# Optimization experiments

Hardware: AMD Instinct MI355X
Metric: run time of the kernel (lower is better)

## Reference

```python
import jax, jax.numpy as jnp
import numpy as np

B, L, D = 8, 2048, 64

def setup_inputs() -> dict:
    key = jax.random.key(0)
    kq, kk, kv, kqm, kkm = jax.random.split(key, 5)
    return {
        "query": jax.random.normal(kq, (B, L, D), dtype=jnp.float32),
        "key": jax.random.normal(kk, (B, L, D), dtype=jnp.float32),
        "value": jax.random.normal(kv, (B, L, D), dtype=jnp.float32),
        "q_mask": jax.random.randint(kqm, (B, L), 0, 2, dtype=jnp.int32),
        "k_mask": jax.random.randint(kkm, (B, L), 0, 2, dtype=jnp.int32),
    }

def reference(query, key, value, q_mask, k_mask):
    # scale defaults to D_q; divide scores by sqrt(D_q)
    D_q = query.shape[-1]
    qm = q_mask.astype(jnp.float32)  # [B, L_q]
    km = k_mask.astype(jnp.float32)  # [B, L_k]
    # outer-product mask: [B, L_q, L_k]
    mask = qm[:, :, None] * km[:, None, :]
    scores = jnp.einsum("bqd,bkd->bqk", query, key) / jnp.sqrt(jnp.float32(D_q))
    # masked_fill(-inf).exp(): masked positions become exactly 0
    A = jnp.where(mask == 0, 0.0, jnp.exp(scores))  # [B, L_q, L_k]
    # sum clamped to min 1.0 (NOT a standard softmax normalization)
    A_sum = jnp.maximum(A.sum(axis=-1, keepdims=True), 1.0)
    attn = A / A_sum
    return jnp.einsum("bqk,bkd->bqd", attn, value)
```

## Files before the change

### kernel.cpp

```cpp
#include <hip/hip_runtime.h>
#include <hip/hip_bf16.h>
#include <stdint.h>

#define BB 8
#define LL 2048
#define DD 64

typedef short bf16x8 __attribute__((ext_vector_type(8)));
typedef float f32x4 __attribute__((ext_vector_type(4)));
typedef unsigned short ushort_t;
typedef __attribute__((address_space(1))) const unsigned int gas_u32;
typedef __attribute__((address_space(3))) unsigned int las_u32;

__device__ __forceinline__ unsigned pk2(float lo, float hi) {
    union { __hip_bfloat162 h; unsigned u; } c;
    c.h = __float22bfloat162_rn(make_float2(lo, hi));
    return c.u;
}
__device__ __forceinline__ float4 ld4(const float* __restrict__ p) {
    return *reinterpret_cast<const float4*>(p);
}
__device__ __forceinline__ bf16x8 cvt8f(float4 a, float4 b) {
    union { bf16x8 v; unsigned u[4]; } r;
    r.u[0] = pk2(a.x, a.y); r.u[1] = pk2(a.z, a.w);
    r.u[2] = pk2(b.x, b.y); r.u[3] = pk2(b.z, b.w);
    return r.v;
}
__device__ __forceinline__ void glds16(const void* g, void* lds_base_uniform) {
    __builtin_amdgcn_global_load_lds((gas_u32*)g, (las_u32*)lds_base_uniform, 16, 0, 0);
}
__device__ __forceinline__ float bfu2f(unsigned bits) {
    union { unsigned u; float f; } c; c.u = bits << 16; return c.f;
}
__device__ __forceinline__ unsigned f2bf_u(float f) {
    union { float f; unsigned u; } v; v.f = f;
    return (v.u + 0x8000u) >> 16;
}
__device__ __forceinline__ bf16x8 cvt8(const float* __restrict__ p) {
    float4 a = ld4(p), b = ld4(p + 4);
    union { bf16x8 v; unsigned u[4]; } r;
    r.u[0] = f2bf_u(a.x) | (f2bf_u(a.y) << 16);
    r.u[1] = f2bf_u(a.z) | (f2bf_u(a.w) << 16);
    r.u[2] = f2bf_u(b.x) | (f2bf_u(b.y) << 16);
    r.u[3] = f2bf_u(b.z) | (f2bf_u(b.w) << 16);
    return r.v;
}

__global__ __launch_bounds__(256) void pack_k_bf16(const float* __restrict__ K,
                                                   ushort_t* __restrict__ Kb) {
    size_t i = ((size_t)blockIdx.x * 256 + threadIdx.x) * 8;
    float4 a = ld4(K + i), b = ld4(K + i + 4);
    uint4 o = { pk2(a.x, a.y), pk2(a.z, a.w), pk2(b.x, b.y), pk2(b.z, b.w) };
    *reinterpret_cast<uint4*>(Kb + i) = o;
}

__global__ __launch_bounds__(256) void transpose_v_bf(const float* __restrict__ V,
                                                      ushort_t* __restrict__ VT) {
    __shared__ float t[64][65];
    const int b  = blockIdx.x >> 5;
    const int kt = (blockIdx.x & 31) << 6;
    {
        const int r  = threadIdx.x >> 2;
        const int cq = (threadIdx.x & 3) << 4;
        const float* src = V + ((size_t)(b * LL + kt + r)) * DD + cq;
        #pragma unroll
        for (int i = 0; i < 4; ++i) {
            float4 v = ld4(src + 4 * i);
            t[r][cq + 4 * i + 0] = v.x; t[r][cq + 4 * i + 1] = v.y;
            t[r][cq + 4 * i + 2] = v.z; t[r][cq + 4 * i + 3] = v.w;
        }
    }
    __syncthreads();
    {
        const int d  = threadIdx.x >> 2;
        const int kq = (threadIdx.x & 3) << 4;
        ushort_t* dst = VT + ((size_t)(b * DD + d)) * LL + kt + kq;
        #pragma unroll
        for (int u = 0; u < 2; ++u) {
            uint4 o;
            o.x = pk2(t[kq + 8 * u + 0][d], t[kq + 8 * u + 1][d]);
            o.y = pk2(t[kq + 8 * u + 2][d], t[kq + 8 * u + 3][d]);
            o.z = pk2(t[kq + 8 * u + 4][d], t[kq + 8 * u + 5][d]);
            o.w = pk2(t[kq + 8 * u + 6][d], t[kq + 8 * u + 7][d]);
            *reinterpret_cast<uint4*>(dst + 8 * u) = o;
        }
    }
}

__global__ __launch_bounds__(512, 4) void attn7(
    const float* __restrict__ Q,
    const ushort_t* __restrict__ Kbf,
    const ushort_t* __restrict__ VTb,
    const int* __restrict__ qmask,
    const int* __restrict__ kmask,
    float* __restrict__ Out)
{
    const int tid  = threadIdx.x;
    const int wave = tid >> 6;
    const int lane = tid & 63;
    const int ln   = lane & 15;
    const int quad = lane >> 4;
    const int s    = wave >> 2;
    const int h    = wave & 3;

    const int b  = blockIdx.x >> 6;
    const int q0 = (blockIdx.x & 63) << 5;

    __shared__ char     lds[2][32768];
    __shared__ ushort_t kmbf[LL];
    __shared__ float    Osum[32][68];
    __shared__ float    Dsum[32];

    const char* Kg = (const char*)Kbf + (size_t)b * LL * DD * 2;
    const char* Vg = (const char*)VTb + (size_t)b * DD * LL * 2;
    const int krow1 = wave * 8 + (lane >> 3);
    const int kscol = (lane & 7) ^ (lane >> 3);
    const int vd1   = wave * 4 + (lane >> 4);
    const int vscol = (lane & 15) ^ (vd1 & 15);

    #define STAGE(buf, k0)                                                      \
        do {                                                                    \
            glds16(Kg + (size_t)((k0) + krow1) * 128 + kscol * 16,              \
                   &lds[buf][wave * 1024]);                                     \
            glds16(Kg + (size_t)((k0) + krow1 + 64) * 128 + kscol * 16,         \
                   &lds[buf][(wave + 8) * 1024]);                               \
            glds16(Vg + (size_t)vd1 * (LL * 2) + (k0) * 2 + vscol * 16,         \
                   &lds[buf][16384 + wave * 1024]);                             \
            glds16(Vg + (size_t)(vd1 + 32) * (LL * 2) + (k0) * 2 + vscol * 16,  \
                   &lds[buf][16384 + (wave + 8) * 1024]);                       \
        } while (0)

    STAGE(0, 0);

    for (int i = tid; i < 32 * 68; i += 512) (&Osum[0][0])[i] = 0.f;
    if (tid < 32) Dsum[tid] = 0.f;
    {
        int4 a = *reinterpret_cast<const int4*>(kmask + b * LL + tid * 4);
        uint2 u;
        u.x = (a.x ? 0x3F80u : 0u) | ((a.y ? 0x3F80u : 0u) << 16);
        u.y = (a.z ? 0x3F80u : 0u) | ((a.w ? 0x3F80u : 0u) << 16);
        *reinterpret_cast<uint2*>(kmbf + tid * 4) = u;
    }
    bf16x8 qf[2];
    {
        const float* qp = Q + ((size_t)(b * LL + q0 + 16 * s + ln)) * DD + quad * 8;
        qf[0] = cvt8f(ld4(qp),      ld4(qp + 4));
        qf[1] = cvt8f(ld4(qp + 32), ld4(qp + 36));
    }

    f32x4 Oacc[4] = {{0,0,0,0},{0,0,0,0},{0,0,0,0},{0,0,0,0}};
    float dsum = 0.f;

    const int src0 = ln + ((quad & 1) << 5);
    const int src1 = src0 + 16;
    const bool hi  = quad >= 2;
    const float EC = 0.125f * 1.44269504f;

    for (int it = 0; it < 16; ++it) {
        __syncthreads();
        if (it != 15) STAGE((it + 1) & 1, (it + 1) * 128);

        const int   k0 = it * 128;
        const char* LK = lds[it & 1];
        const char* LV = lds[it & 1] + 16384;

        bf16x8 kf[2][2];
        #pragma unroll
        for (int tt = 0; tt < 2; ++tt) {
            const int r = 32 * h + 16 * tt + ln;
            #pragma unroll
            for (int dh = 0; dh < 2; ++dh) {
                const int c = (dh * 4 + quad) ^ (ln & 7);
                kf[tt][dh] = *reinterpret_cast<const bf16x8*>(LK + r * 128 + c * 16);
            }
        }
        bf16x8 vf[4];
        #pragma unroll
        for (int db = 0; db < 4; ++db) {
            const int d = db * 16 + ln;
            const int c = (4 * h + quad) ^ ln;
            vf[db] = *reinterpret_cast<const bf16x8*>(LV + d * 256 + c * 16);
        }
        float4 fm[2];
        #pragma unroll
        for (int tt = 0; tt < 2; ++tt) {
            ushort4 mu = *reinterpret_cast<const ushort4*>(
                kmbf + k0 + 32 * h + 16 * tt + 4 * quad);
            fm[tt] = make_float4(bfu2f(mu.x), bfu2f(mu.y), bfu2f(mu.z), bfu2f(mu.w));
        }

        unsigned w[2][2];
        #pragma unroll
        for (int tt = 0; tt < 2; ++tt) {
            f32x4 acc = (f32x4){0.f, 0.f, 0.f, 0.f};
            acc = __builtin_amdgcn_mfma_f32_16x16x32_bf16(kf[tt][0], qf[0], acc, 0, 0, 0);
            acc = __builtin_amdgcn_mfma_f32_16x16x32_bf16(kf[tt][1], qf[1], acc, 0, 0, 0);
            float e0 = exp2f(acc[0] * EC) * fm[tt].x;
            float e1 = exp2f(acc[1] * EC) * fm[tt].y;
            float e2 = exp2f(acc[2] * EC) * fm[tt].z;
            float e3 = exp2f(acc[3] * EC) * fm[tt].w;
            dsum += (e0 + e1) + (e2 + e3);
            w[tt][0] = pk2(e0, e1);
            w[tt][1] = pk2(e2, e3);
        }
        union { bf16x8 v; unsigned u[4]; } pf;
        {
            unsigned a0 = __shfl(w[0][0], src0), b0 = __shfl(w[1][0], src0);
            unsigned a1 = __shfl(w[0][1], src0), b1 = __shfl(w[1][1], src0);
            unsigned a2 = __shfl(w[0][0], src1), b2 = __shfl(w[1][0], src1);
            unsigned a3 = __shfl(w[0][1], src1), b3 = __shfl(w[1][1], src1);
            pf.u[0] = hi ? b0 : a0;
            pf.u[1] = hi ? b1 : a1;
            pf.u[2] = hi ? b2 : a2;
            pf.u[3] = hi ? b3 : a3;
        }
        #pragma unroll
        for (int db = 0; db < 4; ++db)
            Oacc[db] = __builtin_amdgcn_mfma_f32_16x16x32_bf16(pf.v, vf[db], Oacc[db], 0, 0, 0);
    }
    #undef STAGE

    {
        float v = dsum;
        v += __shfl_xor(v, 16);
        v += __shfl_xor(v, 32);
        dsum = v;
    }

    #pragma unroll
    for (int db = 0; db < 4; ++db)
        #pragma unroll
        for (int r = 0; r < 4; ++r)
            atomicAdd(&Osum[16 * s + quad * 4 + r][db * 16 + ln], Oacc[db][r]);
    if (quad == 0) atomicAdd(&Dsum[16 * s + ln], dsum);
    __syncthreads();

    const int q  = tid >> 4;
    const int d0 = (tid & 15) << 2;
    float dn  = Dsum[q];
    float inv = 1.0f / fmaxf(dn, 1.0f);
    float sc  = qmask[b * LL + q0 + q] ? inv : 0.0f;
    f32x4 o = *reinterpret_cast<const f32x4*>(&Osum[q][d0]) * sc;
    float* op = Out + ((size_t)(b * LL + q0 + q)) * DD + d0;
    *reinterpret_cast<f32x4*>(op) = o;
}

__global__ __launch_bounds__(256, 4) void attn_mfma(
    const float* __restrict__ Q, const float* __restrict__ K,
    const float* __restrict__ V, const int* __restrict__ qmask,
    const int* __restrict__ kmask, float* __restrict__ Out)
{
    const int tid  = threadIdx.x;
    const int wave = tid >> 6;
    const int lane = tid & 63;
    const int n    = lane & 15;
    const int quad = lane >> 4;
    const int bx = blockIdx.x;
    const int b  = bx >> 7;
    const int q0 = (bx & 127) << 4;
    __shared__ float Pl[4][576];
    __shared__ float Opart[4][16][68];
    __shared__ float Denp[4][16];
    const float* Qp = Q + ((size_t)(b * LL + q0 + n)) * DD + quad * 8;
    bf16x8 qf0 = cvt8(Qp);
    bf16x8 qf1 = cvt8(Qp + 32);
    const float* Kb = K + ((size_t)(b * LL) + n) * DD + quad * 8;
    const float* Vb = V + ((size_t)(b * LL) + quad * 8) * DD + n;
    const int* kmb = kmask + b * LL;
    f32x4 Oacc[4] = {{0,0,0,0},{0,0,0,0},{0,0,0,0},{0,0,0,0}};
    float den[4]  = {0.f, 0.f, 0.f, 0.f};
    float*       pw = &Pl[wave][144 * (n >> 3) + 36 * quad + (n & 7)];
    const float* pr = &Pl[wave][9 * lane];
    const int kbeg = wave * (LL / 4);
    const int kend = kbeg + (LL / 4);
    for (int k0 = kbeg; k0 < kend; k0 += 32) {
        const float* krow = Kb + (size_t)k0 * DD;
        bf16x8 kA0 = cvt8(krow);
        bf16x8 kA1 = cvt8(krow + 32);
        bf16x8 kB0 = cvt8(krow + 16 * DD);
        bf16x8 kB1 = cvt8(krow + 16 * DD + 32);
        f32x4 z = {0.f, 0.f, 0.f, 0.f};
        f32x4 S0 = __builtin_amdgcn_mfma_f32_16x16x32_bf16(qf0, kA0, z, 0, 0, 0);
        S0 = __builtin_amdgcn_mfma_f32_16x16x32_bf16(qf1, kA1, S0, 0, 0, 0);
        f32x4 S1 = __builtin_amdgcn_mfma_f32_16x16x32_bf16(qf0, kB0, z, 0, 0, 0);
        S1 = __builtin_amdgcn_mfma_f32_16x16x32_bf16(qf1, kB1, S1, 0, 0, 0);
        float km0 = (float)kmb[k0 + n];
        float km1 = (float)kmb[k0 + 16 + n];
        #pragma unroll
        for (int r = 0; r < 4; ++r) {
            float e0 = __expf(S0[r] * 0.125f) * km0;
            float e1 = __expf(S1[r] * 0.125f) * km1;
            den[r] += e0 + e1;
            pw[9 * r]       = e0;
            pw[288 + 9 * r] = e1;
        }
        __builtin_amdgcn_wave_barrier();
        float pv[8];
        #pragma unroll
        for (int j = 0; j < 8; ++j) pv[j] = pr[j];
        __builtin_amdgcn_wave_barrier();
        union { bf16x8 v; unsigned u[4]; } pf;
        #pragma unroll
        for (int j = 0; j < 4; ++j)
            pf.u[j] = f2bf_u(pv[2 * j]) | (f2bf_u(pv[2 * j + 1]) << 16);
        const float* vrow = Vb + (size_t)k0 * DD;
        #pragma unroll
        for (int db = 0; db < 4; ++db) {
            union { bf16x8 v; unsigned u[4]; } vfr;
            #pragma unroll
            for (int jj = 0; jj < 4; ++jj) {
                unsigned lo  = f2bf_u(vrow[(2 * jj) * DD + db * 16]);
                unsigned hi2 = f2bf_u(vrow[(2 * jj + 1) * DD + db * 16]);
                vfr.u[jj] = lo | (hi2 << 16);
            }
            Oacc[db] = __builtin_amdgcn_mfma_f32_16x16x32_bf16(pf.v, vfr.v, Oacc[db], 0, 0, 0);
        }
    }
    #pragma unroll
    for (int r = 0; r < 4; ++r) {
        float v = den[r];
        v += __shfl_xor(v, 1); v += __shfl_xor(v, 2);
        v += __shfl_xor(v, 4); v += __shfl_xor(v, 8);
        den[r] = v;
    }
    #pragma unroll
    for (int db = 0; db < 4; ++db)
        #pragma unroll
        for (int r = 0; r < 4; ++r)
            Opart[wave][quad * 4 + r][db * 16 + n] = Oacc[db][r];
    if (n == 0) {
        #pragma unroll
        for (int r = 0; r < 4; ++r) Denp[wave][quad * 4 + r] = den[r];
    }
    __syncthreads();
    const int q  = tid >> 4;
    const int d0 = (tid & 15) * 4;
    f32x4 sum = *reinterpret_cast<const f32x4*>(&Opart[0][q][d0]);
    sum += *reinterpret_cast<const f32x4*>(&Opart[1][q][d0]);
    sum += *reinterpret_cast<const f32x4*>(&Opart[2][q][d0]);
    sum += *reinterpret_cast<const f32x4*>(&Opart[3][q][d0]);
    float dn  = Denp[0][q] + Denp[1][q] + Denp[2][q] + Denp[3][q];
    float inv = 1.0f / fmaxf(dn, 1.0f);
    float s   = qmask[b * LL + q0 + q] ? inv : 0.0f;
    f32x4 o   = sum * s;
    float* op = Out + ((size_t)(b * LL + q0 + q)) * DD + d0;
    *reinterpret_cast<f32x4*>(op) = o;
}

extern "C" void kernel_launch(void* const* d_in, const int* in_sizes, int n_in,
                              void* d_out, int out_size, void* d_ws, size_t ws_size,
                              hipStream_t stream) {
    (void)in_sizes; (void)n_in; (void)out_size;
    const float* Q  = (const float*)d_in[0];
    const float* K  = (const float*)d_in[1];
    const float* V  = (const float*)d_in[2];
    const int* qm   = (const int*)d_in[3];
    const int* km   = (const int*)d_in[4];
    float* Out      = (float*)d_out;

    const size_t elems    = (size_t)BB * LL * DD;
    const size_t ws_need  = elems * 2 * sizeof(ushort_t);
    if (ws_size >= ws_need && d_ws != nullptr) {
        ushort_t* Kbf = (ushort_t*)d_ws;
        ushort_t* VTb = Kbf + elems;
        pack_k_bf16   <<<dim3(elems / (256 * 8)), dim3(256), 0, stream>>>(K, Kbf);
        transpose_v_bf<<<dim3(BB * (LL / 64)),    dim3(256), 0, stream>>>(V, VTb);
        attn7<<<dim3(BB * (LL / 32)), dim3(512), 0, stream>>>(Q, Kbf, VTb, qm, km, Out);
    } else {
        attn_mfma<<<dim3(BB * (LL / 16)), dim3(256), 0, stream>>>(Q, K, V, qm, km, Out);
    }
}
```

Before: 117.5 us.

## Split attention over key ranges with larger query tiles and a separate reduce kernel

```diff
diff --git a/kernel.cpp b/kernel.cpp
--- a/kernel.cpp
+++ b/kernel.cpp
@@ -87,55 +87,46 @@
     }
 }
 
-__global__ __launch_bounds__(512, 4) void attn7(
+__global__ __launch_bounds__(512, 4) void attn8(
     const float* __restrict__ Q,
     const ushort_t* __restrict__ Kbf,
     const ushort_t* __restrict__ VTb,
-    const int* __restrict__ qmask,
     const int* __restrict__ kmask,
-    float* __restrict__ Out)
+    float* __restrict__ Opart)
 {
     const int tid  = threadIdx.x;
     const int wave = tid >> 6;
     const int lane = tid & 63;
     const int ln   = lane & 15;
     const int quad = lane >> 4;
-    const int s    = wave >> 2;
-    const int h    = wave & 3;
-
-    const int b  = blockIdx.x >> 6;
-    const int q0 = (blockIdx.x & 63) << 5;
-
-    __shared__ char     lds[2][32768];
-    __shared__ ushort_t kmbf[LL];
-    __shared__ float    Osum[32][68];
-    __shared__ float    Dsum[32];
+
+    const int bx    = blockIdx.x;
+    const int ksp   = bx & 3;
+    const int qt    = (bx >> 2) & 15;
+    const int b     = bx >> 6;
+    const int q0    = qt * 128;
+    const int kbase = ksp * 512;
+
+    __shared__ char     lds[2][16384];
+    __shared__ ushort_t kmbf[512];
 
     const char* Kg = (const char*)Kbf + (size_t)b * LL * DD * 2;
     const char* Vg = (const char*)VTb + (size_t)b * DD * LL * 2;
-    const int krow1 = wave * 8 + (lane >> 3);
-    const int kscol = (lane & 7) ^ (lane >> 3);
-    const int vd1   = wave * 4 + (lane >> 4);
-    const int vscol = (lane & 15) ^ (vd1 & 15);
-
-    #define STAGE(buf, k0)                                                      \
-        do {                                                                    \
-            glds16(Kg + (size_t)((k0) + krow1) * 128 + kscol * 16,              \
-                   &lds[buf][wave * 1024]);                                     \
-            glds16(Kg + (size_t)((k0) + krow1 + 64) * 128 + kscol * 16,         \
-                   &lds[buf][(wave + 8) * 1024]);                               \
-            glds16(Vg + (size_t)vd1 * (LL * 2) + (k0) * 2 + vscol * 16,         \
-                   &lds[buf][16384 + wave * 1024]);                             \
-            glds16(Vg + (size_t)(vd1 + 32) * (LL * 2) + (k0) * 2 + vscol * 16,  \
-                   &lds[buf][16384 + (wave + 8) * 1024]);                       \
+    const int gr = tid >> 3;
+    const int gc = (tid & 7) ^ (gr & 7);
+
+    #define STAGE(buf, k0)                                                     \
+        do {                                                                   \
+            glds16(Kg + (size_t)(kbase + (k0) + gr) * 128 + gc * 16,           \
+                   &lds[buf][wave * 1024]);                                    \
+            glds16(Vg + (size_t)gr * (LL * 2) + (kbase + (k0)) * 2 + gc * 16,  \
+                   &lds[buf][8192 + wave * 1024]);                             \
         } while (0)
 
     STAGE(0, 0);
 
-    for (int i = tid; i < 32 * 68; i += 512) (&Osum[0][0])[i] = 0.f;
-    if (tid < 32) Dsum[tid] = 0.f;
-    {
-        int4 a = *reinterpret_cast<const int4*>(kmask + b * LL + tid * 4);
+    if (tid < 128) {
+        int4 a = *reinterpret_cast<const int4*>(kmask + b * LL + kbase + tid * 4);
         uint2 u;
         u.x = (a.x ? 0x3F80u : 0u) | ((a.y ? 0x3F80u : 0u) << 16);
         u.y = (a.z ? 0x3F80u : 0u) | ((a.w ? 0x3F80u : 0u) << 16);
@@ -143,7 +134,7 @@
     }
     bf16x8 qf[2];
     {
-        const float* qp = Q + ((size_t)(b * LL + q0 + 16 * s + ln)) * DD + quad * 8;
+        const float* qp = Q + ((size_t)(b * LL + q0 + 16 * wave + ln)) * DD + quad * 8;
         qf[0] = cvt8f(ld4(qp),      ld4(qp + 4));
         qf[1] = cvt8f(ld4(qp + 32), ld4(qp + 36));
     }
@@ -156,67 +147,65 @@
     const bool hi  = quad >= 2;
     const float EC = 0.125f * 1.44269504f;
 
-    for (int it = 0; it < 16; ++it) {
+    for (int it = 0; it < 8; ++it) {
         __syncthreads();
-        if (it != 15) STAGE((it + 1) & 1, (it + 1) * 128);
-
-        const int   k0 = it * 128;
+        if (it != 7) STAGE((it + 1) & 1, (it + 1) * 64);
+
         const char* LK = lds[it & 1];
-        const char* LV = lds[it & 1] + 16384;
-
-        bf16x8 kf[2][2];
-        #pragma unroll
-        for (int tt = 0; tt < 2; ++tt) {
-            const int r = 32 * h + 16 * tt + ln;
+        const char* LV = lds[it & 1] + 8192;
+
+        bf16x8 kf[4][2];
+        #pragma unroll
+        for (int tt = 0; tt < 4; ++tt) {
+            const int r = 16 * tt + ln;
             #pragma unroll
             for (int dh = 0; dh < 2; ++dh) {
                 const int c = (dh * 4 + quad) ^ (ln & 7);
                 kf[tt][dh] = *reinterpret_cast<const bf16x8*>(LK + r * 128 + c * 16);
             }
         }
-        bf16x8 vf[4];
-        #pragma unroll
-        for (int db = 0; db < 4; ++db) {
-            const int d = db * 16 + ln;
-            const int c = (4 * h + quad) ^ ln;
-            vf[db] = *reinterpret_cast<const bf16x8*>(LV + d * 256 + c * 16);
-        }
-        float4 fm[2];
-        #pragma unroll
-        for (int tt = 0; tt < 2; ++tt) {
-            ushort4 mu = *reinterpret_cast<const ushort4*>(
-                kmbf + k0 + 32 * h + 16 * tt + 4 * quad);
-            fm[tt] = make_float4(bfu2f(mu.x), bfu2f(mu.y), bfu2f(mu.z), bfu2f(mu.w));
-        }
-
-        unsigned w[2][2];
-        #pragma unroll
-        for (int tt = 0; tt < 2; ++tt) {
+        bf16x8 vf[2][4];
+        #pragma unroll
+        for (int kh = 0; kh < 2; ++kh) {
+            const int c = (kh * 4 + quad) ^ (ln & 7);
+            #pragma unroll
+            for (int db = 0; db < 4; ++db) {
+                const int d = db * 16 + ln;
+                vf[kh][db] = *reinterpret_cast<const bf16x8*>(LV + d * 128 + c * 16);
+            }
+        }
+
+        unsigned w[4][2];
+        #pragma unroll
+        for (int tt = 0; tt < 4; ++tt) {
             f32x4 acc = (f32x4){0.f, 0.f, 0.f, 0.f};
             acc = __builtin_amdgcn_mfma_f32_16x16x32_bf16(kf[tt][0], qf[0], acc, 0, 0, 0);
             acc = __builtin_amdgcn_mfma_f32_16x16x32_bf16(kf[tt][1], qf[1], acc, 0, 0, 0);
-            float e0 = exp2f(acc[0] * EC) * fm[tt].x;
-            float e1 = exp2f(acc[1] * EC) * fm[tt].y;
-            float e2 = exp2f(acc[2] * EC) * fm[tt].z;
-            float e3 = exp2f(acc[3] * EC) * fm[tt].w;
+            ushort4 mu = *reinterpret_cast<const ushort4*>(
+                kmbf + it * 64 + 16 * tt + 4 * quad);
+            float e0 = exp2f(acc[0] * EC) * bfu2f(mu.x);
+            float e1 = exp2f(acc[1] * EC) * bfu2f(mu.y);
+            float e2 = exp2f(acc[2] * EC) * bfu2f(mu.z);
+            float e3 = exp2f(acc[3] * EC) * bfu2f(mu.w);
             dsum += (e0 + e1) + (e2 + e3);
             w[tt][0] = pk2(e0, e1);
             w[tt][1] = pk2(e2, e3);
         }
-        union { bf16x8 v; unsigned u[4]; } pf;
-        {
-            unsigned a0 = __shfl(w[0][0], src0), b0 = __shfl(w[1][0], src0);
-            unsigned a1 = __shfl(w[0][1], src0), b1 = __shfl(w[1][1], src0);
-            unsigned a2 = __shfl(w[0][0], src1), b2 = __shfl(w[1][0], src1);
-            unsigned a3 = __shfl(w[0][1], src1), b3 = __shfl(w[1][1], src1);
+        #pragma unroll
+        for (int g = 0; g < 2; ++g) {
+            union { bf16x8 v; unsigned u[4]; } pf;
+            unsigned a0 = __shfl(w[2*g][0], src0), b0 = __shfl(w[2*g+1][0], src0);
+            unsigned a1 = __shfl(w[2*g][1], src0), b1 = __shfl(w[2*g+1][1], src0);
+            unsigned a2 = __shfl(w[2*g][0], src1), b2 = __shfl(w[2*g+1][0], src1);
+            unsigned a3 = __shfl(w[2*g][1], src1), b3 = __shfl(w[2*g+1][1], src1);
             pf.u[0] = hi ? b0 : a0;
             pf.u[1] = hi ? b1 : a1;
             pf.u[2] = hi ? b2 : a2;
             pf.u[3] = hi ? b3 : a3;
-        }
-        #pragma unroll
-        for (int db = 0; db < 4; ++db)
-            Oacc[db] = __builtin_amdgcn_mfma_f32_16x16x32_bf16(pf.v, vf[db], Oacc[db], 0, 0, 0);
+            #pragma unroll
+            for (int db = 0; db < 4; ++db)
+                Oacc[db] = __builtin_amdgcn_mfma_f32_16x16x32_bf16(pf.v, vf[g][db], Oacc[db], 0, 0, 0);
+        }
     }
     #undef STAGE
 
@@ -227,22 +216,45 @@
         dsum = v;
     }
 
+    float* pb = Opart + (size_t)bx * 8320;
     #pragma unroll
     for (int db = 0; db < 4; ++db)
         #pragma unroll
         for (int r = 0; r < 4; ++r)
-            atomicAdd(&Osum[16 * s + quad * 4 + r][db * 16 + ln], Oacc[db][r]);
-    if (quad == 0) atomicAdd(&Dsum[16 * s + ln], dsum);
-    __syncthreads();
-
-    const int q  = tid >> 4;
-    const int d0 = (tid & 15) << 2;
-    float dn  = Dsum[q];
-    float inv = 1.0f / fmaxf(dn, 1.0f);
-    float sc  = qmask[b * LL + q0 + q] ? inv : 0.0f;
-    f32x4 o = *reinterpret_cast<const f32x4*>(&Osum[q][d0]) * sc;
-    float* op = Out + ((size_t)(b * LL + q0 + q)) * DD + d0;
-    *reinterpret_cast<f32x4*>(op) = o;
+            pb[(16 * wave + quad * 4 + r) * 64 + db * 16 + ln] = Oacc[db][r];
+    if (quad == 0) pb[8192 + 16 * wave + ln] = dsum;
+}
+
+__global__ __launch_bounds__(256) void reduce_norm(
+    const float* __restrict__ Opart,
+    const int* __restrict__ qmask,
+    float* __restrict__ Out)
+{
+    const int rb = blockIdx.x;
+    const int qt = rb & 15;
+    const int b  = rb >> 4;
+    const int t  = threadIdx.x;
+    const int q  = t >> 1;
+    const int d0 = (t & 1) * 32;
+
+    const float* p0 = Opart + (size_t)((b * 16 + qt) * 4 + 0) * 8320;
+    const float* p1 = p0 + 8320;
+    const float* p2 = p1 + 8320;
+    const float* p3 = p2 + 8320;
+
+    float dn = p0[8192 + q] + p1[8192 + q] + p2[8192 + q] + p3[8192 + q];
+    float sc = qmask[b * LL + qt * 128 + q] ? (1.0f / fmaxf(dn, 1.0f)) : 0.0f;
+
+    const int off = q * 64 + d0;
+    float* op = Out + ((size_t)(b * LL + qt * 128 + q)) * DD + d0;
+    #pragma unroll
+    for (int i = 0; i < 8; ++i) {
+        f32x4 v = *reinterpret_cast<const f32x4*>(p0 + off + 4 * i)
+                + *reinterpret_cast<const f32x4*>(p1 + off + 4 * i)
+                + *reinterpret_cast<const f32x4*>(p2 + off + 4 * i)
+                + *reinterpret_cast<const f32x4*>(p3 + off + 4 * i);
+        *reinterpret_cast<f32x4*>(op + 4 * i) = v * sc;
+    }
 }
 
 __global__ __launch_bounds__(256, 4) void attn_mfma(
@@ -259,7 +271,7 @@
     const int b  = bx >> 7;
     const int q0 = (bx & 127) << 4;
     __shared__ float Pl[4][576];
-    __shared__ float Opart[4][16][68];
+    __shared__ float Opart2[4][16][68];
     __shared__ float Denp[4][16];
     const float* Qp = Q + ((size_t)(b * LL + q0 + n)) * DD + quad * 8;
     bf16x8 qf0 = cvt8(Qp);
@@ -327,7 +339,7 @@
     for (int db = 0; db < 4; ++db)
         #pragma unroll
         for (int r = 0; r < 4; ++r)
-            Opart[wave][quad * 4 + r][db * 16 + n] = Oacc[db][r];
+            Opart2[wave][quad * 4 + r][db * 16 + n] = Oacc[db][r];
     if (n == 0) {
         #pragma unroll
         for (int r = 0; r < 4; ++r) Denp[wave][quad * 4 + r] = den[r];
@@ -335,10 +347,10 @@
     __syncthreads();
     const int q  = tid >> 4;
     const int d0 = (tid & 15) * 4;
-    f32x4 sum = *reinterpret_cast<const f32x4*>(&Opart[0][q][d0]);
-    sum += *reinterpret_cast<const f32x4*>(&Opart[1][q][d0]);
-    sum += *reinterpret_cast<const f32x4*>(&Opart[2][q][d0]);
-    sum += *reinterpret_cast<const f32x4*>(&Opart[3][q][d0]);
+    f32x4 sum = *reinterpret_cast<const f32x4*>(&Opart2[0][q][d0]);
+    sum += *reinterpret_cast<const f32x4*>(&Opart2[1][q][d0]);
+    sum += *reinterpret_cast<const f32x4*>(&Opart2[2][q][d0]);
+    sum += *reinterpret_cast<const f32x4*>(&Opart2[3][q][d0]);
     float dn  = Denp[0][q] + Denp[1][q] + Denp[2][q] + Denp[3][q];
     float inv = 1.0f / fmaxf(dn, 1.0f);
     float s   = qmask[b * LL + q0 + q] ? inv : 0.0f;
@@ -358,14 +370,17 @@
     const int* km   = (const int*)d_in[4];
     float* Out      = (float*)d_out;
 
-    const size_t elems    = (size_t)BB * LL * DD;
-    const size_t ws_need  = elems * 2 * sizeof(ushort_t);
+    const size_t elems   = (size_t)BB * LL * DD;
+    const size_t part_off = 4u * 1024 * 1024;
+    const size_t ws_need  = part_off + (size_t)512 * 8320 * sizeof(float);
     if (ws_size >= ws_need && d_ws != nullptr) {
         ushort_t* Kbf = (ushort_t*)d_ws;
         ushort_t* VTb = Kbf + elems;
+        float* Opart  = (float*)((char*)d_ws + part_off);
         pack_k_bf16   <<<dim3(elems / (256 * 8)), dim3(256), 0, stream>>>(K, Kbf);
         transpose_v_bf<<<dim3(BB * (LL / 64)),    dim3(256), 0, stream>>>(V, VTb);
-        attn7<<<dim3(BB * (LL / 32)), dim3(512), 0, stream>>>(Q, Kbf, VTb, qm, km, Out);
+        attn8<<<dim3(512), dim3(512), 0, stream>>>(Q, Kbf, VTb, km, Opart);
+        reduce_norm<<<dim3(128), dim3(256), 0, stream>>>(Opart, qm, Out);
     } else {
         attn_mfma<<<dim3(BB * (LL / 16)), dim3(256), 0, stream>>>(Q, K, V, qm, km, Out);
     }
```

Result: faster. 106.2 us (-9.6%).
